# Kernel optimization log

Measured on AMD Instinct MI355X. Metric: run time of the kernel, lower is better.

## Reference

```python
import jax, jax.numpy as jnp
import numpy as np

SR = 48000
SEG = 960
NH = 8
BASE = 440.0
F0_MIN = 20.0
F0_MAX = 16000.0
EPS = 1e-4
N, C, LF = 16, 256, 200


def _interp_linear(x, Lw):
    # Matches torch F.interpolate(mode='linear', align_corners=False).
    # x: (N, C, Lf) -> (N, C, Lw)
    Lf = x.shape[-1]
    scale = Lf / Lw
    src = (jnp.arange(Lw, dtype=x.dtype) + 0.5) * scale - 0.5
    src = jnp.clip(src, 0.0, Lf - 1)
    i0 = jnp.floor(src).astype(jnp.int32)
    i1 = jnp.minimum(i0 + 1, Lf - 1)
    w = src - i0.astype(x.dtype)
    return x[..., i0] * (1.0 - w) + x[..., i1] * w


def setup_inputs() -> dict:
    key = jax.random.key(0)
    ks = jax.random.split(key, 7)
    scale = 1.0 / np.sqrt(C)
    return {
        "x": jax.random.normal(ks[0], (N, C, LF), dtype=jnp.float32),
        "mag_w": jax.random.uniform(ks[1], (NH, C), jnp.float32, -scale, scale),
        "mag_b": jax.random.uniform(ks[2], (NH,), jnp.float32, -scale, scale),
        "cn_scale": jnp.ones((1, C, 1), jnp.float32),
        "cn_shift": jnp.zeros((1, C, 1), jnp.float32),
        "oct_w": jax.random.uniform(ks[3], (1, C), jnp.float32, -scale, scale),
        "oct_b": jax.random.uniform(ks[4], (1,), jnp.float32, -scale, scale),
    }


def reference(x, mag_w, mag_b, cn_scale, cn_shift, oct_w, oct_b):
    n, c, Lf = x.shape
    Lw = Lf * SEG
    # ChannelNorm (torch.std is unbiased -> ddof=1)
    mu = jnp.mean(x, axis=1, keepdims=True)
    sigma = jnp.std(x, axis=1, keepdims=True, ddof=1) + EPS
    xn = (x - mu) / sigma * cn_scale + cn_shift
    # 1x1 convs
    octave = jnp.einsum('ncl,oc->nol', xn, oct_w) + oct_b[None, :, None]  # (N,1,Lf)
    mag = jnp.exp(jnp.minimum(jnp.einsum('ncl,hc->nhl', x, mag_w) + mag_b[None, :, None], 6.0))  # (N,NH,Lf)
    f0 = jnp.clip(BASE * jnp.exp2(octave), F0_MIN, F0_MAX)  # (N,1,Lf)
    mul = jnp.arange(1, NH + 1, dtype=x.dtype)[None, :, None]
    formants = f0 * mul  # (N,NH,Lf)
    formants_w = _interp_linear(formants, Lw)  # (N,NH,Lw)
    mag_w_up = _interp_linear(mag, Lw)         # (N,NH,Lw)
    t = jnp.cumsum(formants_w / SR, axis=2)
    harmonics = jnp.sin(2.0 * jnp.pi * t) * mag_w_up
    wave = jnp.mean(harmonics, axis=1, keepdims=True)  # (N,1,Lw)
    return wave
```

## Files before the change

kernel.cpp:

```cpp
#include <hip/hip_runtime.h>
#include <math.h>


#define NB   16
#define CCH  256
#define LFR  200
#define LW   192000
#define NHH  8
#define NKM  201
#define CG   8
#define CPB  32
#define INV_SR (1.0 / 48000.0)
#define TPB  4
#define KMB  ((NKM + TPB - 1) / TPB)

__device__ inline double wave_sum64(double v) {
    #pragma unroll
    for (int off = 32; off > 0; off >>= 1) v += __shfl_xor(v, off);
    return v;
}
__device__ inline double wave_incl_scan64(double v) {
    int lane = threadIdx.x & 63;
    #pragma unroll
    for (int off = 1; off < 64; off <<= 1) {
        double t = __shfl_up(v, off);
        if (lane >= off) v += t;
    }
    return v;
}

__global__ __launch_bounds__(256)
void hg_partial(const float* __restrict__ x,
                const float* __restrict__ mag_w,
                const float* __restrict__ cn_scale,
                const float* __restrict__ oct_w,
                double* __restrict__ ps, double* __restrict__ ps2,
                double* __restrict__ pdx, float* __restrict__ pmg) {
    int n = blockIdx.x, cg = blockIdx.y;
    int t = threadIdx.x;
    const float* xb = x + (size_t)n * CCH * LFR;
    int cbase = cg * CPB;

    double s = 0.0, s2 = 0.0, dx = 0.0;
    float zm[NHH] = {0.f, 0.f, 0.f, 0.f, 0.f, 0.f, 0.f, 0.f};
    #pragma unroll 8
    for (int cc = 0; cc < CPB; cc++) {
        int c = cbase + cc;
        float xf = (t < LFR) ? xb[(size_t)c * LFR + t] : 0.f;
        double xd = (double)xf;
        double w2 = (double)cn_scale[c] * (double)oct_w[c];
        s += xd;
        s2 = fma(xd, xd, s2);
        dx = fma(xd, w2, dx);
        #pragma unroll
        for (int h = 0; h < NHH; h++)
            zm[h] = fmaf(xf, mag_w[h * CCH + c], zm[h]);
    }
    size_t pi = ((size_t)n * CG + cg) * 256 + t;
    ps[pi] = s; ps2[pi] = s2; pdx[pi] = dx;
    #pragma unroll
    for (int h = 0; h < NHH; h++)
        pmg[(((size_t)n * CG + cg) * NHH + h) * 256 + t] = zm[h];
}

__global__ __launch_bounds__(256)
void hg_wave(const double* __restrict__ ps, const double* __restrict__ ps2,
             const double* __restrict__ pdx, const float* __restrict__ pmg,
             const float* __restrict__ mag_b,
             const float* __restrict__ cn_scale, const float* __restrict__ cn_shift,
             const float* __restrict__ oct_w, const float* __restrict__ oct_b,
             float* __restrict__ out) {
    __shared__ double Fl[LFR];
    __shared__ double Tl[LFR];
    __shared__ float  Mgl[LFR][NHH];
    __shared__ double SAB[2];

    int n = blockIdx.y;
    int tid = threadIdx.x;

    if (tid < 64) {
        double sa = 0.0, sb = 0.0;
        #pragma unroll
        for (int k = 0; k < 4; k++) {
            int c = tid + 64 * k;
            double ow = (double)oct_w[c];
            sa = fma((double)cn_scale[c], ow, sa);
            sb = fma((double)cn_shift[c], ow, sb);
        }
        sa = wave_sum64(sa);
        sb = wave_sum64(sb);
        if (tid == 0) { SAB[0] = sa; SAB[1] = sb; }
    }
    __syncthreads();

    if (tid < LFR) {
        double s_ = 0.0, s2_ = 0.0, dx_ = 0.0;
        #pragma unroll
        for (int cg2 = 0; cg2 < CG; cg2++) {
            size_t pj = ((size_t)n * CG + cg2) * 256 + tid;
            s_ += ps[pj]; s2_ += ps2[pj]; dx_ += pdx[pj];
        }
        double mu  = s_ * (1.0 / 256.0);
        double var = (s2_ - s_ * mu) * (1.0 / 255.0);
        double inv = 1.0 / (sqrt(var) + 1e-4);
        double oct = inv * (dx_ - mu * SAB[0]) + SAB[1] + (double)oct_b[0];
        double f0  = 440.0 * exp2(oct);
        Fl[tid] = fmin(fmax(f0, 20.0), 16000.0);
        #pragma unroll
        for (int h = 0; h < NHH; h++) {
            float z = 0.f;
            #pragma unroll
            for (int cg2 = 0; cg2 < CG; cg2++)
                z += pmg[(((size_t)n * CG + cg2) * NHH + h) * 256 + tid];
            Mgl[tid][h] = 0.125f * expf(fminf(z + mag_b[h], 6.f));
        }
    }
    __syncthreads();

    if (tid < 64) {
        double carry = 480.0 * Fl[0];
        for (int base = 0; base < LFR; base += 64) {
            int k = base + tid;
            double d = (k < LFR - 1) ? 480.0 * (Fl[k] + Fl[k + 1]) : 0.0;
            double scn = wave_incl_scan64(d);
            if (k < LFR) Tl[k] = carry + scn - d;
            carry += __shfl(scn, 63);
        }
    }
    __syncthreads();

    #pragma unroll
    for (int i = 0; i < TPB; i++) {
        int km = blockIdx.x * TPB + i;
        if (km >= NKM) break;
        int kc = min(max(km - 1, 0), LFR - 1);
        bool body = (km >= 1 && km <= LFR - 1);
        double Sd = Fl[kc] * INV_SR;
        double Qd = body ? (Fl[km] - Fl[km - 1]) * (INV_SR / 1920.0) : 0.0;
        double Pd = (km == 0) ? (-480.0 * Fl[0] * INV_SR) : Tl[km - 1] * INV_SR;
        double Pp = Pd + 480.0 * Sd + 230400.0 * Qd;
        double Sp = Sd + 960.0 * Qd;
        float Pf = (float)(Pp - floor(Pp));
        float Sf = (float)Sp;
        float Qf = (float)Qd;
        float ma[NHH], md[NHH];
        #pragma unroll
        for (int h = 0; h < NHH; h++) {
            float a = Mgl[kc][h];
            ma[h] = a;
            md[h] = body ? (Mgl[km][h] - a) : 0.f;
        }

        if (tid < 240) {
            int j0 = 960 * km - 480 + tid * 4;
            if (j0 >= 0 && j0 < LW) {
                float r[4];
                #pragma unroll
                for (int u = 0; u < 4; u++) {
                    float pc = (float)(tid * 4 - 479 + u);
                    float tb = fmaf(pc, fmaf(Qf, pc, Sf), Pf);
                    float fr, s1, c1;
                    asm("v_fract_f32 %0, %1" : "=v"(fr) : "v"(tb));
                    asm("v_sin_f32 %0, %1" : "=v"(s1) : "v"(fr));
                    asm("v_cos_f32 %0, %1" : "=v"(c1) : "v"(fr));
                    float twoc = c1 + c1;
                    float w = (pc + 479.5f) * (1.0f / 960.0f);
                    float sp = 0.f, sc = s1;
                    float acc = 0.f;
                    #pragma unroll
                    for (int h = 0; h < NHH; h++) {
                        acc = fmaf(fmaf(md[h], w, ma[h]), sc, acc);
                        float sn = fmaf(twoc, sc, -sp);
                        sp = sc; sc = sn;
                    }
                    r[u] = acc;
                }
                *(float4*)(out + (size_t)n * LW + j0) =
                    make_float4(r[0], r[1], r[2], r[3]);
            }
        }
    }
}

extern "C" void kernel_launch(void* const* d_in, const int* in_sizes, int n_in,
                              void* d_out, int out_size, void* d_ws, size_t ws_size,
                              hipStream_t stream) {
    const float* x        = (const float*)d_in[0];
    const float* mag_w    = (const float*)d_in[1];
    const float* mag_b    = (const float*)d_in[2];
    const float* cn_scale = (const float*)d_in[3];
    const float* cn_shift = (const float*)d_in[4];
    const float* oct_w    = (const float*)d_in[5];
    const float* oct_b    = (const float*)d_in[6];
    float* out = (float*)d_out;

    double* ps  = (double*)d_ws;
    double* ps2 = ps  + (size_t)NB * CG * 256;
    double* pdx = ps2 + (size_t)NB * CG * 256;
    float*  pmg = (float*)(pdx + (size_t)NB * CG * 256);

    hg_partial<<<dim3(NB, CG), dim3(256), 0, stream>>>(
        x, mag_w, cn_scale, oct_w, ps, ps2, pdx, pmg);
    hg_wave<<<dim3(KMB, NB), dim3(256), 0, stream>>>(
        ps, ps2, pdx, pmg, mag_b, cn_scale, cn_shift, oct_w, oct_b, out);
}
```

Before: 24.49 us.

## Fuse partial reduction and wave synthesis into one 1024-thread kernel

Merges the channel-statistics kernel and the waveform kernel into a single launch. Each block of 1024 threads recomputes the full per-frame channel sums for its batch item in shared memory across four channel groups. It computes the magnitude projection only for the 16 frames its 13 segments need. This removes one kernel launch and the global workspace round trip. In exchange, every one of the 16 blocks per batch item redundantly re-reads the whole 256x200 input slab and repeats the f0 scan.

```diff
diff --git a/kernel.cpp b/kernel.cpp
--- a/kernel.cpp
+++ b/kernel.cpp
@@ -8,11 +8,10 @@
 #define LW   192000
 #define NHH  8
 #define NKM  201
-#define CG   8
-#define CPB  32
+#define RPB  13
+#define NKG  16
+#define NF   16
 #define INV_SR (1.0 / 48000.0)
-#define TPB  4
-#define KMB  ((NKM + TPB - 1) / TPB)
 
 __device__ inline double wave_sum64(double v) {
     #pragma unroll
@@ -29,91 +28,89 @@
     return v;
 }
 
-__global__ __launch_bounds__(256)
-void hg_partial(const float* __restrict__ x,
-                const float* __restrict__ mag_w,
-                const float* __restrict__ cn_scale,
-                const float* __restrict__ oct_w,
-                double* __restrict__ ps, double* __restrict__ ps2,
-                double* __restrict__ pdx, float* __restrict__ pmg) {
-    int n = blockIdx.x, cg = blockIdx.y;
-    int t = threadIdx.x;
-    const float* xb = x + (size_t)n * CCH * LFR;
-    int cbase = cg * CPB;
-
-    double s = 0.0, s2 = 0.0, dx = 0.0;
-    float zm[NHH] = {0.f, 0.f, 0.f, 0.f, 0.f, 0.f, 0.f, 0.f};
-    #pragma unroll 8
-    for (int cc = 0; cc < CPB; cc++) {
-        int c = cbase + cc;
-        float xf = (t < LFR) ? xb[(size_t)c * LFR + t] : 0.f;
-        double xd = (double)xf;
-        double w2 = (double)cn_scale[c] * (double)oct_w[c];
-        s += xd;
-        s2 = fma(xd, xd, s2);
-        dx = fma(xd, w2, dx);
-        #pragma unroll
-        for (int h = 0; h < NHH; h++)
-            zm[h] = fmaf(xf, mag_w[h * CCH + c], zm[h]);
-    }
-    size_t pi = ((size_t)n * CG + cg) * 256 + t;
-    ps[pi] = s; ps2[pi] = s2; pdx[pi] = dx;
-    #pragma unroll
-    for (int h = 0; h < NHH; h++)
-        pmg[(((size_t)n * CG + cg) * NHH + h) * 256 + t] = zm[h];
-}
-
-__global__ __launch_bounds__(256)
-void hg_wave(const double* __restrict__ ps, const double* __restrict__ ps2,
-             const double* __restrict__ pdx, const float* __restrict__ pmg,
-             const float* __restrict__ mag_b,
-             const float* __restrict__ cn_scale, const float* __restrict__ cn_shift,
-             const float* __restrict__ oct_w, const float* __restrict__ oct_b,
-             float* __restrict__ out) {
+__global__ __launch_bounds__(1024)
+void hg_all(const float* __restrict__ x,
+            const float* __restrict__ mag_w, const float* __restrict__ mag_b,
+            const float* __restrict__ cn_scale, const float* __restrict__ cn_shift,
+            const float* __restrict__ oct_w, const float* __restrict__ oct_b,
+            float* __restrict__ out) {
+    __shared__ double w2l[CCH];
+    __shared__ double psum[4][256], psumsq[4][256], pdotx[4][256];
+    __shared__ float  pmag[4][NF][NHH];
     __shared__ double Fl[LFR];
     __shared__ double Tl[LFR];
-    __shared__ float  Mgl[LFR][NHH];
+    __shared__ float  Mgl[NF][NHH];
     __shared__ double SAB[2];
 
-    int n = blockIdx.y;
+    int kg = blockIdx.x, n = blockIdx.y;
     int tid = threadIdx.x;
+    int t = tid & 255;
+    int g = tid >> 8;
+    int fbase = max(kg * RPB - 1, 0);
 
-    if (tid < 64) {
+    if (tid < CCH)
+        w2l[tid] = (double)cn_scale[tid] * (double)oct_w[tid];
+    if (tid >= 960) {
+        int lane = tid & 63;
         double sa = 0.0, sb = 0.0;
         #pragma unroll
         for (int k = 0; k < 4; k++) {
-            int c = tid + 64 * k;
+            int c = lane + 64 * k;
             double ow = (double)oct_w[c];
             sa = fma((double)cn_scale[c], ow, sa);
             sb = fma((double)cn_shift[c], ow, sb);
         }
         sa = wave_sum64(sa);
         sb = wave_sum64(sb);
-        if (tid == 0) { SAB[0] = sa; SAB[1] = sb; }
+        if (lane == 0) { SAB[0] = sa; SAB[1] = sb; }
+    }
+    __syncthreads();
+
+    int gs = __builtin_amdgcn_readfirstlane(g);
+    const float* xb = x + (size_t)n * CCH * LFR;
+    int nf = t - fbase;
+    bool needmag = (t < LFR) && ((unsigned)nf < (unsigned)NF);
+
+    double s = 0.0, s2 = 0.0, dx = 0.0;
+    float zm[NHH] = {0.f, 0.f, 0.f, 0.f, 0.f, 0.f, 0.f, 0.f};
+    #pragma unroll 4
+    for (int cc = 0; cc < 64; cc++) {
+        int c = gs * 64 + cc;
+        float xf = (t < LFR) ? xb[(size_t)c * LFR + t] : 0.f;
+        double xd = (double)xf;
+        s  += xd;
+        s2  = fma(xd, xd, s2);
+        dx  = fma(xd, w2l[c], dx);
+        if (needmag) {
+            #pragma unroll
+            for (int h = 0; h < NHH; h++)
+                zm[h] = fmaf(xf, mag_w[h * CCH + c], zm[h]);
+        }
+    }
+    psum[g][t] = s; psumsq[g][t] = s2; pdotx[g][t] = dx;
+    if (needmag) {
+        #pragma unroll
+        for (int h = 0; h < NHH; h++) pmag[g][nf][h] = zm[h];
     }
     __syncthreads();
 
     if (tid < LFR) {
-        double s_ = 0.0, s2_ = 0.0, dx_ = 0.0;
-        #pragma unroll
-        for (int cg2 = 0; cg2 < CG; cg2++) {
-            size_t pj = ((size_t)n * CG + cg2) * 256 + tid;
-            s_ += ps[pj]; s2_ += ps2[pj]; dx_ += pdx[pj];
-        }
+        double s_  = psum[0][tid] + psum[1][tid] + psum[2][tid] + psum[3][tid];
+        double s2_ = psumsq[0][tid] + psumsq[1][tid] + psumsq[2][tid] + psumsq[3][tid];
+        double dx_ = pdotx[0][tid] + pdotx[1][tid] + pdotx[2][tid] + pdotx[3][tid];
         double mu  = s_ * (1.0 / 256.0);
         double var = (s2_ - s_ * mu) * (1.0 / 255.0);
         double inv = 1.0 / (sqrt(var) + 1e-4);
         double oct = inv * (dx_ - mu * SAB[0]) + SAB[1] + (double)oct_b[0];
         double f0  = 440.0 * exp2(oct);
         Fl[tid] = fmin(fmax(f0, 20.0), 16000.0);
-        #pragma unroll
-        for (int h = 0; h < NHH; h++) {
-            float z = 0.f;
-            #pragma unroll
-            for (int cg2 = 0; cg2 < CG; cg2++)
-                z += pmg[(((size_t)n * CG + cg2) * NHH + h) * 256 + tid];
-            Mgl[tid][h] = 0.125f * expf(fminf(z + mag_b[h], 6.f));
-        }
+    }
+    if (tid >= 256 && tid < 256 + NF * NHH) {
+        int q = tid - 256;
+        int w = q >> 3, h = q & 7;
+        float z = pmag[0][w][h] + pmag[1][w][h] + pmag[2][w][h] + pmag[3][w][h]
+                + mag_b[h];
+        Mgl[w][h] = 0.125f * expf(fminf(z, 6.f));
     }
     __syncthreads();
 
@@ -129,10 +126,11 @@
     }
     __syncthreads();
 
-    #pragma unroll
-    for (int i = 0; i < TPB; i++) {
-        int km = blockIdx.x * TPB + i;
-        if (km >= NKM) break;
+    int sub = tid >> 8;
+    int tt  = tid & 255;
+    for (int i = sub; i < RPB; i += 4) {
+        int km = kg * RPB + i;
+        if (km >= NKM) continue;
         int kc = min(max(km - 1, 0), LFR - 1);
         bool body = (km >= 1 && km <= LFR - 1);
         double Sd = Fl[kc] * INV_SR;
@@ -143,21 +141,22 @@
         float Pf = (float)(Pp - floor(Pp));
         float Sf = (float)Sp;
         float Qf = (float)Qd;
+        int nfc = kc - fbase;
         float ma[NHH], md[NHH];
         #pragma unroll
         for (int h = 0; h < NHH; h++) {
-            float a = Mgl[kc][h];
+            float a = Mgl[nfc][h];
             ma[h] = a;
-            md[h] = body ? (Mgl[km][h] - a) : 0.f;
+            md[h] = body ? (Mgl[km - fbase][h] - a) : 0.f;
         }
 
-        if (tid < 240) {
-            int j0 = 960 * km - 480 + tid * 4;
+        if (tt < 240) {
+            int j0 = 960 * km - 480 + tt * 4;
             if (j0 >= 0 && j0 < LW) {
                 float r[4];
                 #pragma unroll
                 for (int u = 0; u < 4; u++) {
-                    float pc = (float)(tid * 4 - 479 + u);
+                    float pc = (float)(tt * 4 - 479 + u);
                     float tb = fmaf(pc, fmaf(Qf, pc, Sf), Pf);
                     float fr, s1, c1;
                     asm("v_fract_f32 %0, %1" : "=v"(fr) : "v"(tb));
@@ -194,13 +193,6 @@
     const float* oct_b    = (const float*)d_in[6];
     float* out = (float*)d_out;
 
-    double* ps  = (double*)d_ws;
-    double* ps2 = ps  + (size_t)NB * CG * 256;
-    double* pdx = ps2 + (size_t)NB * CG * 256;
-    float*  pmg = (float*)(pdx + (size_t)NB * CG * 256);
-
-    hg_partial<<<dim3(NB, CG), dim3(256), 0, stream>>>(
-        x, mag_w, cn_scale, oct_w, ps, ps2, pdx, pmg);
-    hg_wave<<<dim3(KMB, NB), dim3(256), 0, stream>>>(
-        ps, ps2, pdx, pmg, mag_b, cn_scale, cn_shift, oct_w, oct_b, out);
+    hg_all<<<dim3(NKG, NB), dim3(1024), 0, stream>>>(
+        x, mag_w, mag_b, cn_scale, cn_shift, oct_w, oct_b, out);
 }
```

Measured after the change: 25.41 us. 3.7% more time.
